# Optimization experiments

Hardware: AMD Instinct MI355X
Metric: run time of the kernel (lower is better)

Reference implementation:

```python
import jax, jax.numpy as jnp
import numpy as np

B, IN, H, OUT = 32768, 64, 256, 768
HM, TS = 4, 64  # hm_modalities, timestep_size; OUT = 3*HM*TS


def setup_inputs() -> dict:
    key = jax.random.key(0)
    ks = jax.random.split(key, 24)
    def w(k, shape):
        scale = 1.0 / np.sqrt(shape[0])
        return jax.random.normal(k, shape, jnp.float32) * scale
    inp = jax.random.normal(ks[0], (B, IN), jnp.float32)
    state1 = jax.random.normal(ks[1], (B, 2 * H), jnp.float32)
    state2 = jax.random.normal(ks[2], (B, 2 * H), jnp.float32)
    d = {"inp": inp, "state1": state1, "state2": state2}
    names = ["wf", "wk", "wi", "ws"]
    for i, n in enumerate(names):
        d[f"l1_{n}"] = w(ks[3 + i], (IN + H, H))
        d[f"l1_b{n[1]}"] = jnp.zeros((H,), jnp.float32)
        d[f"l2_{n}"] = w(ks[7 + i], (H + H, H))
        d[f"l2_b{n[1]}"] = jnp.zeros((H,), jnp.float32)
    d["ff_w"] = w(ks[11], (H, OUT))
    return d


def lstm_cell(state, x_in, wf, bf, wk, bk, wi, bi, ws, bs):
    h = wf.shape[1]
    prev_out = state[:, :h]
    cell = state[:, h:]
    x = jnp.concatenate([x_in, prev_out], axis=1)
    reset = jax.nn.sigmoid(x @ wf + bf)
    write = jax.nn.sigmoid(x @ wk + bk)
    interm = jnp.tanh(x @ wi + bi)
    read = jax.nn.sigmoid(x @ ws + bs)
    cell = reset * cell + write * interm
    out = read * jnp.tanh(cell)
    return out, jnp.concatenate([out, cell], axis=1)


def reference(inp, state1, state2,
              l1_wf, l1_bf, l1_wk, l1_bk, l1_wi, l1_bi, l1_ws, l1_bs,
              l2_wf, l2_bf, l2_wk, l2_bk, l2_wi, l2_bi, l2_ws, l2_bs,
              ff_w):
    out, new_state1 = lstm_cell(state1, inp, l1_wf, l1_bf, l1_wk, l1_bk,
                                l1_wi, l1_bi, l1_ws, l1_bs)
    out, new_state2 = lstm_cell(state2, out, l2_wf, l2_bf, l2_wk, l2_bk,
                                l2_wi, l2_bi, l2_ws, l2_bs)
    out = out @ ff_w  # [B, OUT]
    third = OUT // 3
    means = out[:, :third]
    deviances = jnp.exp(out[:, third:2 * third])
    mult = out[:, -third:].reshape(B, HM, TS)
    mult = jax.nn.softmax(mult, axis=1).reshape(B, HM * TS)
    return means, deviances, mult, new_state1, new_state2
```

## Files before the change

### kernel.cpp

```cpp
#include <hip/hip_runtime.h>


typedef __attribute__((ext_vector_type(8))) short short8;
typedef __attribute__((ext_vector_type(4))) short short4_t;
typedef __attribute__((ext_vector_type(4))) float floatx4;

#define BATCH 32768

static const size_t DEV_OFF  = (size_t)BATCH * 256;
static const size_t MULT_OFF = (size_t)2 * BATCH * 256;
static const size_t NS1_OFF  = (size_t)3 * BATCH * 256;
static const size_t NS2_OFF  = NS1_OFF + (size_t)BATCH * 512;

static const size_t W1P = 0;
static const size_t W2P = (size_t)1024 * 320;
static const size_t W3P = W2P + (size_t)1024 * 512;
static const size_t X1O = W3P + (size_t)768 * 256;
static const size_t X2O = X1O + (size_t)BATCH * 320;
static const size_t X3O = X2O + (size_t)BATCH * 512;

__device__ __forceinline__ unsigned short f2bf(float f) {
    union { float f; unsigned int i; } v; v.f = f;
    unsigned int i = v.i;
    i += 0x7fff + ((i >> 16) & 1);
    return (unsigned short)(i >> 16);
}
__device__ __forceinline__ float sigmoidf_(float x) {
    return 1.f / (1.f + __expf(-x));
}
__device__ __forceinline__ float tanhf_(float x) {
    float e = __expf(2.f * x);
    return 1.f - 2.f / (e + 1.f);
}

__device__ __forceinline__ void gl_lds16(const unsigned short* g,
                                         unsigned short* l) {
    __builtin_amdgcn_global_load_lds(
        (const __attribute__((address_space(1))) unsigned int*)g,
        (__attribute__((address_space(3))) unsigned int*)l,
        16, 0, 0);
}

__global__ __launch_bounds__(256) void pack_all(
    const float* __restrict__ inp, const float* __restrict__ s1,
    const float* __restrict__ s2,
    const float* __restrict__ w10, const float* __restrict__ w11,
    const float* __restrict__ w12, const float* __restrict__ w13,
    const float* __restrict__ w20, const float* __restrict__ w21,
    const float* __restrict__ w22, const float* __restrict__ w23,
    const float* __restrict__ fw, unsigned short* __restrict__ ws)
{
    const int q = blockIdx.x * 256 + threadIdx.x;
    if (q < 524288) {
        int r = q >> 4, c = (q & 15) << 2;
        float4 v = *(const float4*)(inp + (size_t)r * 64 + c);
        short4_t h;
        h.x = (short)f2bf(v.x); h.y = (short)f2bf(v.y);
        h.z = (short)f2bf(v.z); h.w = (short)f2bf(v.w);
        *(short4_t*)(ws + X1O + (size_t)r * 320 + c) = h;
    } else if (q < 2621440) {
        int j = q - 524288;
        int r = j >> 6, c = (j & 63) << 2;
        float4 v = *(const float4*)(s1 + (size_t)r * 512 + c);
        short4_t h;
        h.x = (short)f2bf(v.x); h.y = (short)f2bf(v.y);
        h.z = (short)f2bf(v.z); h.w = (short)f2bf(v.w);
        *(short4_t*)(ws + X1O + (size_t)r * 320 + 64 + c) = h;
    } else if (q < 4718592) {
        int j = q - 2621440;
        int r = j >> 6, c = (j & 63) << 2;
        float4 v = *(const float4*)(s2 + (size_t)r * 512 + c);
        short4_t h;
        h.x = (short)f2bf(v.x); h.y = (short)f2bf(v.y);
        h.z = (short)f2bf(v.z); h.w = (short)f2bf(v.w);
        *(short4_t*)(ws + X2O + (size_t)r * 512 + 256 + c) = h;
    } else if (q < 4800512) {
        int j = q - 4718592;
        int n = j / 80, k = (j % 80) << 2;
        int hh = ((n >> 6) << 4) + (n & 15);
        int g = (n >> 4) & 3;
        const float* s = g == 0 ? w10 : g == 1 ? w11 : g == 2 ? w12 : w13;
        short4_t o;
        o.x = (short)f2bf(s[(size_t)(k + 0) * 256 + hh]);
        o.y = (short)f2bf(s[(size_t)(k + 1) * 256 + hh]);
        o.z = (short)f2bf(s[(size_t)(k + 2) * 256 + hh]);
        o.w = (short)f2bf(s[(size_t)(k + 3) * 256 + hh]);
        *(short4_t*)(ws + W1P + (size_t)n * 320 + k) = o;
    } else if (q < 4931584) {
        int j = q - 4800512;
        int n = j >> 7, k = (j & 127) << 2;
        int hh = ((n >> 6) << 4) + (n & 15);
        int g = (n >> 4) & 3;
        const float* s = g == 0 ? w20 : g == 1 ? w21 : g == 2 ? w22 : w23;
        short4_t o;
        o.x = (short)f2bf(s[(size_t)(k + 0) * 256 + hh]);
        o.y = (short)f2bf(s[(size_t)(k + 1) * 256 + hh]);
        o.z = (short)f2bf(s[(size_t)(k + 2) * 256 + hh]);
        o.w = (short)f2bf(s[(size_t)(k + 3) * 256 + hh]);
        *(short4_t*)(ws + W2P + (size_t)n * 512 + k) = o;
    } else {
        int j = q - 4931584;
        int n = j >> 6, k = (j & 63) << 2;
        int col;
        if (n < 512) col = n;
        else {
            int t = (((n - 512) >> 6) << 4) + (n & 15);
            int m = (n >> 4) & 3;
            col = 512 + m * 64 + t;
        }
        short4_t o;
        o.x = (short)f2bf(fw[(size_t)(k + 0) * 768 + col]);
        o.y = (short)f2bf(fw[(size_t)(k + 1) * 768 + col]);
        o.z = (short)f2bf(fw[(size_t)(k + 2) * 768 + col]);
        o.w = (short)f2bf(fw[(size_t)(k + 3) * 768 + col]);
        *(short4_t*)(ws + W3P + (size_t)n * 256 + k) = o;
    }
}

template<int KT, int XST>
__global__ __launch_bounds__(256) void lstm_gemm(
    const unsigned short* __restrict__ xin,
    const unsigned short* __restrict__ wp,
    const float* __restrict__ b0, const float* __restrict__ b1,
    const float* __restrict__ b2, const float* __restrict__ b3,
    const float* __restrict__ state,
    float* __restrict__ nstate,
    unsigned short* __restrict__ xnext)
{
    __shared__ __align__(16) struct {
        unsigned short a[128][64];
        unsigned short b[128][64];
    } lds;

    const int tid  = threadIdx.x;
    const int w    = tid >> 6;
    const int lane = tid & 63;
    const int lhi  = lane >> 4, llo = lane & 15;
    const int wr   = w >> 1, wc = w & 1;

    const int lin  = blockIdx.x;
    const int xcd  = lin & 7;
    const int kk   = lin >> 3;
    const int nt   = kk & 7;
    const int row0 = (xcd * 32 + (kk >> 3)) * 128;
    const int nc0  = nt * 128;

    const int h = nt * 32 + wc * 16 + llo;
    const float bf_ = b0[h], bk_ = b1[h], bi_ = b2[h], bs_ = b3[h];

    floatx4 acc[4][4];
#pragma unroll
    for (int i = 0; i < 4; i++)
#pragma unroll
        for (int j = 0; j < 4; j++) acc[i][j] = (floatx4){0.f, 0.f, 0.f, 0.f};

    const int arow  = (w << 5) + (lane >> 3);
    const int acolb = (((lane & 7) ^ ((lane >> 3) & 7)) << 3);
    const unsigned short* agp = xin + (size_t)(row0 + arow) * KT + acolb;
    const unsigned short* bgp = wp  + (size_t)(nc0 + arow) * KT + acolb;

    const int sx  = llo & 7;
    const int kq0 = ((lhi ^ sx) << 3);
    const int kq1 = (((4 | lhi) ^ sx) << 3);

    for (int c = 0; c < KT / 64; ++c) {
        const int kb = c << 6;
#pragma unroll
        for (int p = 0; p < 4; ++p) {
            gl_lds16(agp + (size_t)(p * 8) * KT + kb,
                     &lds.a[(w << 5) + (p << 3)][0]);
            gl_lds16(bgp + (size_t)(p * 8) * KT + kb,
                     &lds.b[(w << 5) + (p << 3)][0]);
        }
        __syncthreads();
#pragma unroll
        for (int ks = 0; ks < 2; ++ks) {
            const int kq = ks ? kq1 : kq0;
            short8 a[4], b[4];
#pragma unroll
            for (int mi = 0; mi < 4; mi++)
                a[mi] = *(const short8*)&lds.a[wr * 64 + mi * 16 + llo][kq];
#pragma unroll
            for (int ni = 0; ni < 4; ni++)
                b[ni] = *(const short8*)&lds.b[wc * 64 + ni * 16 + llo][kq];
#pragma unroll
            for (int mi = 0; mi < 4; mi++)
#pragma unroll
                for (int ni = 0; ni < 4; ni++)
                    acc[mi][ni] = __builtin_amdgcn_mfma_f32_16x16x32_bf16(
                        a[mi], b[ni], acc[mi][ni], 0, 0, 0);
        }
        __syncthreads();
    }

#pragma unroll
    for (int mi = 0; mi < 4; mi++)
#pragma unroll
        for (int r = 0; r < 4; r++) {
            const int m = wr * 64 + mi * 16 + lhi * 4 + r;
            const size_t rowel = (size_t)(row0 + m) * 512;
            float rst = sigmoidf_(acc[mi][0][r] + bf_);
            float wrt = sigmoidf_(acc[mi][1][r] + bk_);
            float itm = tanhf_(acc[mi][2][r] + bi_);
            float rd  = sigmoidf_(acc[mi][3][r] + bs_);
            float cold = state[rowel + 256 + h];
            float cell = rst * cold + wrt * itm;
            float o = rd * tanhf_(cell);
            nstate[rowel + h]       = o;
            nstate[rowel + 256 + h] = cell;
            xnext[(size_t)(row0 + m) * XST + h] = f2bf(o);
        }
}

__global__ __launch_bounds__(256) void ff_gemm(
    const unsigned short* __restrict__ xin,
    const unsigned short* __restrict__ wp,
    float* __restrict__ out)
{
    __shared__ __align__(16) struct {
        unsigned short a[128][64];
        unsigned short b[128][64];
    } lds;

    const int tid  = threadIdx.x;
    const int w    = tid >> 6;
    const int lane = tid & 63;
    const int lhi  = lane >> 4, llo = lane & 15;
    const int wr   = w >> 1, wc = w & 1;

    const int lin  = blockIdx.x;
    const int xcd  = lin & 7;
    const int kk   = lin >> 3;
    const int nt   = kk % 6;
    const int row0 = (xcd * 32 + kk / 6) * 128;
    const int nc0  = nt * 128;

    floatx4 acc[4][4];
#pragma unroll
    for (int i = 0; i < 4; i++)
#pragma unroll
        for (int j = 0; j < 4; j++) acc[i][j] = (floatx4){0.f, 0.f, 0.f, 0.f};

    const int arow  = (w << 5) + (lane >> 3);
    const int acolb = (((lane & 7) ^ ((lane >> 3) & 7)) << 3);
    const unsigned short* agp = xin + (size_t)(row0 + arow) * 256 + acolb;
    const unsigned short* bgp = wp  + (size_t)(nc0 + arow) * 256 + acolb;

    const int sx  = llo & 7;
    const int kq0 = ((lhi ^ sx) << 3);
    const int kq1 = (((4 | lhi) ^ sx) << 3);

    for (int c = 0; c < 4; ++c) {
        const int kb = c << 6;
#pragma unroll
        for (int p = 0; p < 4; ++p) {
            gl_lds16(agp + (size_t)(p * 8) * 256 + kb,
                     &lds.a[(w << 5) + (p << 3)][0]);
            gl_lds16(bgp + (size_t)(p * 8) * 256 + kb,
                     &lds.b[(w << 5) + (p << 3)][0]);
        }
        __syncthreads();
#pragma unroll
        for (int ks = 0; ks < 2; ++ks) {
            const int kq = ks ? kq1 : kq0;
            short8 a[4], b[4];
#pragma unroll
            for (int mi = 0; mi < 4; mi++)
                a[mi] = *(const short8*)&lds.a[wr * 64 + mi * 16 + llo][kq];
#pragma unroll
            for (int ni = 0; ni < 4; ni++)
                b[ni] = *(const short8*)&lds.b[wc * 64 + ni * 16 + llo][kq];
#pragma unroll
            for (int mi = 0; mi < 4; mi++)
#pragma unroll
                for (int ni = 0; ni < 4; ni++)
                    acc[mi][ni] = __builtin_amdgcn_mfma_f32_16x16x32_bf16(
                        a[mi], b[ni], acc[mi][ni], 0, 0, 0);
        }
        __syncthreads();
    }

    if (nt < 4) {
        const bool dev = (nt >= 2);
        float* obase = out + (dev ? DEV_OFF : (size_t)0);
        const int cb = (nt & 1) * 128 + wc * 64;
#pragma unroll
        for (int mi = 0; mi < 4; mi++)
#pragma unroll
            for (int ni = 0; ni < 4; ni++) {
                const int cc = cb + ni * 16 + llo;
#pragma unroll
                for (int r = 0; r < 4; r++) {
                    const int m = wr * 64 + mi * 16 + lhi * 4 + r;
                    float v = acc[mi][ni][r];
                    if (dev) v = __expf(v);
                    obase[(size_t)(row0 + m) * 256 + cc] = v;
                }
            }
    } else {
        const int t = (nt - 4) * 32 + wc * 16 + llo;
#pragma unroll
        for (int mi = 0; mi < 4; mi++)
#pragma unroll
            for (int r = 0; r < 4; r++) {
                const int mrow = wr * 64 + mi * 16 + lhi * 4 + r;
                float v0 = acc[mi][0][r], v1 = acc[mi][1][r];
                float v2 = acc[mi][2][r], v3 = acc[mi][3][r];
                float mx = fmaxf(fmaxf(v0, v1), fmaxf(v2, v3));
                float e0 = __expf(v0 - mx), e1 = __expf(v1 - mx);
                float e2 = __expf(v2 - mx), e3 = __expf(v3 - mx);
                float inv = 1.f / (e0 + e1 + e2 + e3);
                size_t base = MULT_OFF + (size_t)(row0 + mrow) * 256 + t;
                out[base]       = e0 * inv;
                out[base + 64]  = e1 * inv;
                out[base + 128] = e2 * inv;
                out[base + 192] = e3 * inv;
            }
    }
}

extern "C" void kernel_launch(void* const* d_in, const int* in_sizes, int n_in,
                              void* d_out, int out_size, void* d_ws, size_t ws_size,
                              hipStream_t stream)
{
    typedef const float* cfp;
    cfp inp = (cfp)d_in[0];
    cfp st1 = (cfp)d_in[1];
    cfp st2 = (cfp)d_in[2];
    cfp l1w0 = (cfp)d_in[3],  l1w1 = (cfp)d_in[7],  l1w2 = (cfp)d_in[11], l1w3 = (cfp)d_in[15];
    cfp l1b0 = (cfp)d_in[4],  l1b1 = (cfp)d_in[8],  l1b2 = (cfp)d_in[12], l1b3 = (cfp)d_in[16];
    cfp l2w0 = (cfp)d_in[5],  l2w1 = (cfp)d_in[9],  l2w2 = (cfp)d_in[13], l2w3 = (cfp)d_in[17];
    cfp l2b0 = (cfp)d_in[6],  l2b1 = (cfp)d_in[10], l2b2 = (cfp)d_in[14], l2b3 = (cfp)d_in[18];
    cfp ffw = (cfp)d_in[19];

    float* out = (float*)d_out;
    unsigned short* ws = (unsigned short*)d_ws;

    pack_all<<<19456, 256, 0, stream>>>(inp, st1, st2,
                                        l1w0, l1w1, l1w2, l1w3,
                                        l2w0, l2w1, l2w2, l2w3, ffw, ws);

    lstm_gemm<320, 512><<<2048, 256, 0, stream>>>(
        ws + X1O, ws + W1P, l1b0, l1b1, l1b2, l1b3,
        st1, out + NS1_OFF, ws + X2O);

    lstm_gemm<512, 256><<<2048, 256, 0, stream>>>(
        ws + X2O, ws + W2P, l2b0, l2b1, l2b2, l2b3,
        st2, out + NS2_OFF, ws + X3O);

    ff_gemm<<<1536, 256, 0, stream>>>(ws + X3O, ws + W3P, out);
}
```

Baseline: 493.1 us.

## Split packing and overlap layer-2/FF packing with layer-1 GEMM via extra blocks

The single packing kernel is split in two. Layer-1 inputs and weights are packed in a smaller kernel with 4 elements per thread. Packing of state2 and the layer-2/FF weights moves into extra blocks appended to the layer-1 GEMM launch, so that conversion work can run alongside the GEMM blocks. Launch bounds of (256,4) are added to the GEMM kernels to target higher occupancy, at the risk of register spills.

Result: faster. 480.7 us (-2.5%).

```diff
diff --git a/kernel.cpp b/kernel.cpp
--- a/kernel.cpp
+++ b/kernel.cpp
@@ -41,104 +41,121 @@
         16, 0, 0);
 }
 
-__global__ __launch_bounds__(256) void pack_all(
+__global__ __launch_bounds__(256) void pack1(
     const float* __restrict__ inp, const float* __restrict__ s1,
-    const float* __restrict__ s2,
     const float* __restrict__ w10, const float* __restrict__ w11,
     const float* __restrict__ w12, const float* __restrict__ w13,
-    const float* __restrict__ w20, const float* __restrict__ w21,
-    const float* __restrict__ w22, const float* __restrict__ w23,
-    const float* __restrict__ fw, unsigned short* __restrict__ ws)
+    unsigned short* __restrict__ ws)
 {
-    const int q = blockIdx.x * 256 + threadIdx.x;
-    if (q < 524288) {
-        int r = q >> 4, c = (q & 15) << 2;
-        float4 v = *(const float4*)(inp + (size_t)r * 64 + c);
-        short4_t h;
-        h.x = (short)f2bf(v.x); h.y = (short)f2bf(v.y);
-        h.z = (short)f2bf(v.z); h.w = (short)f2bf(v.w);
-        *(short4_t*)(ws + X1O + (size_t)r * 320 + c) = h;
-    } else if (q < 2621440) {
-        int j = q - 524288;
-        int r = j >> 6, c = (j & 63) << 2;
-        float4 v = *(const float4*)(s1 + (size_t)r * 512 + c);
-        short4_t h;
-        h.x = (short)f2bf(v.x); h.y = (short)f2bf(v.y);
-        h.z = (short)f2bf(v.z); h.w = (short)f2bf(v.w);
-        *(short4_t*)(ws + X1O + (size_t)r * 320 + 64 + c) = h;
-    } else if (q < 4718592) {
-        int j = q - 2621440;
-        int r = j >> 6, c = (j & 63) << 2;
-        float4 v = *(const float4*)(s2 + (size_t)r * 512 + c);
-        short4_t h;
-        h.x = (short)f2bf(v.x); h.y = (short)f2bf(v.y);
-        h.z = (short)f2bf(v.z); h.w = (short)f2bf(v.w);
-        *(short4_t*)(ws + X2O + (size_t)r * 512 + 256 + c) = h;
-    } else if (q < 4800512) {
-        int j = q - 4718592;
-        int n = j / 80, k = (j % 80) << 2;
-        int hh = ((n >> 6) << 4) + (n & 15);
-        int g = (n >> 4) & 3;
-        const float* s = g == 0 ? w10 : g == 1 ? w11 : g == 2 ? w12 : w13;
-        short4_t o;
-        o.x = (short)f2bf(s[(size_t)(k + 0) * 256 + hh]);
-        o.y = (short)f2bf(s[(size_t)(k + 1) * 256 + hh]);
-        o.z = (short)f2bf(s[(size_t)(k + 2) * 256 + hh]);
-        o.w = (short)f2bf(s[(size_t)(k + 3) * 256 + hh]);
-        *(short4_t*)(ws + W1P + (size_t)n * 320 + k) = o;
-    } else if (q < 4931584) {
-        int j = q - 4800512;
-        int n = j >> 7, k = (j & 127) << 2;
-        int hh = ((n >> 6) << 4) + (n & 15);
-        int g = (n >> 4) & 3;
-        const float* s = g == 0 ? w20 : g == 1 ? w21 : g == 2 ? w22 : w23;
-        short4_t o;
-        o.x = (short)f2bf(s[(size_t)(k + 0) * 256 + hh]);
-        o.y = (short)f2bf(s[(size_t)(k + 1) * 256 + hh]);
-        o.z = (short)f2bf(s[(size_t)(k + 2) * 256 + hh]);
-        o.w = (short)f2bf(s[(size_t)(k + 3) * 256 + hh]);
-        *(short4_t*)(ws + W2P + (size_t)n * 512 + k) = o;
-    } else {
-        int j = q - 4931584;
-        int n = j >> 6, k = (j & 63) << 2;
-        int col;
-        if (n < 512) col = n;
-        else {
-            int t = (((n - 512) >> 6) << 4) + (n & 15);
-            int m = (n >> 4) & 3;
-            col = 512 + m * 64 + t;
-        }
-        short4_t o;
-        o.x = (short)f2bf(fw[(size_t)(k + 0) * 768 + col]);
-        o.y = (short)f2bf(fw[(size_t)(k + 1) * 768 + col]);
-        o.z = (short)f2bf(fw[(size_t)(k + 2) * 768 + col]);
-        o.w = (short)f2bf(fw[(size_t)(k + 3) * 768 + col]);
-        *(short4_t*)(ws + W3P + (size_t)n * 256 + k) = o;
-    }
-}
-
-template<int KT, int XST>
-__global__ __launch_bounds__(256) void lstm_gemm(
+    const int wt = blockIdx.x * 256 + threadIdx.x;
+#pragma unroll
+    for (int j = 0; j < 4; ++j) {
+        const int q = wt + j * 675840;
+        if (q < 524288) {
+            int r = q >> 4, c = (q & 15) << 2;
+            float4 v = *(const float4*)(inp + (size_t)r * 64 + c);
+            short4_t h;
+            h.x = (short)f2bf(v.x); h.y = (short)f2bf(v.y);
+            h.z = (short)f2bf(v.z); h.w = (short)f2bf(v.w);
+            *(short4_t*)(ws + X1O + (size_t)r * 320 + c) = h;
+        } else if (q < 2621440) {
+            int jj = q - 524288;
+            int r = jj >> 6, c = (jj & 63) << 2;
+            float4 v = *(const float4*)(s1 + (size_t)r * 512 + c);
+            short4_t h;
+            h.x = (short)f2bf(v.x); h.y = (short)f2bf(v.y);
+            h.z = (short)f2bf(v.z); h.w = (short)f2bf(v.w);
+            *(short4_t*)(ws + X1O + (size_t)r * 320 + 64 + c) = h;
+        } else {
+            int jj = q - 2621440;
+            int n = jj / 80, k = (jj % 80) << 2;
+            int hh = ((n >> 6) << 4) + (n & 15);
+            int g = (n >> 4) & 3;
+            const float* s = g == 0 ? w10 : g == 1 ? w11 : g == 2 ? w12 : w13;
+            short4_t o;
+            o.x = (short)f2bf(s[(size_t)(k + 0) * 256 + hh]);
+            o.y = (short)f2bf(s[(size_t)(k + 1) * 256 + hh]);
+            o.z = (short)f2bf(s[(size_t)(k + 2) * 256 + hh]);
+            o.w = (short)f2bf(s[(size_t)(k + 3) * 256 + hh]);
+            *(short4_t*)(ws + W1P + (size_t)n * 320 + k) = o;
+        }
+    }
+}
+
+template<int KT, int XST, bool PACK>
+__global__ __launch_bounds__(256, 4) void lstm_gemm(
     const unsigned short* __restrict__ xin,
     const unsigned short* __restrict__ wp,
     const float* __restrict__ b0, const float* __restrict__ b1,
     const float* __restrict__ b2, const float* __restrict__ b3,
     const float* __restrict__ state,
     float* __restrict__ nstate,
-    unsigned short* __restrict__ xnext)
+    unsigned short* __restrict__ xnext,
+    const float* __restrict__ s2f,
+    const float* __restrict__ w20, const float* __restrict__ w21,
+    const float* __restrict__ w22, const float* __restrict__ w23,
+    const float* __restrict__ fw,
+    unsigned short* __restrict__ wsbase)
 {
+    const int tid = threadIdx.x;
+    const int lin = blockIdx.x;
+
+    if (PACK && lin >= 2048) {
+        const int wt = (lin - 2048) * 256 + tid;
+#pragma unroll
+        for (int j = 0; j < 4; ++j) {
+            const int q = wt + j * 569344;
+            if (q < 2097152) {
+                int r = q >> 6, c = (q & 63) << 2;
+                float4 v = *(const float4*)(s2f + (size_t)r * 512 + c);
+                short4_t h;
+                h.x = (short)f2bf(v.x); h.y = (short)f2bf(v.y);
+                h.z = (short)f2bf(v.z); h.w = (short)f2bf(v.w);
+                *(short4_t*)(wsbase + X2O + (size_t)r * 512 + 256 + c) = h;
+            } else if (q < 2228224) {
+                int jj = q - 2097152;
+                int n = jj >> 7, k = (jj & 127) << 2;
+                int hh = ((n >> 6) << 4) + (n & 15);
+                int g = (n >> 4) & 3;
+                const float* s = g == 0 ? w20 : g == 1 ? w21
+                               : g == 2 ? w22 : w23;
+                short4_t o;
+                o.x = (short)f2bf(s[(size_t)(k + 0) * 256 + hh]);
+                o.y = (short)f2bf(s[(size_t)(k + 1) * 256 + hh]);
+                o.z = (short)f2bf(s[(size_t)(k + 2) * 256 + hh]);
+                o.w = (short)f2bf(s[(size_t)(k + 3) * 256 + hh]);
+                *(short4_t*)(wsbase + W2P + (size_t)n * 512 + k) = o;
+            } else {
+                int jj = q - 2228224;
+                int n = jj >> 6, k = (jj & 63) << 2;
+                int col;
+                if (n < 512) col = n;
+                else {
+                    int t = (((n - 512) >> 6) << 4) + (n & 15);
+                    int m = (n >> 4) & 3;
+                    col = 512 + m * 64 + t;
+                }
+                short4_t o;
+                o.x = (short)f2bf(fw[(size_t)(k + 0) * 768 + col]);
+                o.y = (short)f2bf(fw[(size_t)(k + 1) * 768 + col]);
+                o.z = (short)f2bf(fw[(size_t)(k + 2) * 768 + col]);
+                o.w = (short)f2bf(fw[(size_t)(k + 3) * 768 + col]);
+                *(short4_t*)(wsbase + W3P + (size_t)n * 256 + k) = o;
+            }
+        }
+        return;
+    }
+
     __shared__ __align__(16) struct {
         unsigned short a[128][64];
         unsigned short b[128][64];
     } lds;
 
-    const int tid  = threadIdx.x;
     const int w    = tid >> 6;
     const int lane = tid & 63;
     const int lhi  = lane >> 4, llo = lane & 15;
     const int wr   = w >> 1, wc = w & 1;
 
-    const int lin  = blockIdx.x;
     const int xcd  = lin & 7;
     const int kk   = lin >> 3;
     const int nt   = kk & 7;
@@ -212,7 +229,7 @@
         }
 }
 
-__global__ __launch_bounds__(256) void ff_gemm(
+__global__ __launch_bounds__(256, 4) void ff_gemm(
     const unsigned short* __restrict__ xin,
     const unsigned short* __restrict__ wp,
     float* __restrict__ out)
@@ -336,17 +353,17 @@
     float* out = (float*)d_out;
     unsigned short* ws = (unsigned short*)d_ws;
 
-    pack_all<<<19456, 256, 0, stream>>>(inp, st1, st2,
-                                        l1w0, l1w1, l1w2, l1w3,
-                                        l2w0, l2w1, l2w2, l2w3, ffw, ws);
-
-    lstm_gemm<320, 512><<<2048, 256, 0, stream>>>(
+    pack1<<<2640, 256, 0, stream>>>(inp, st1, l1w0, l1w1, l1w2, l1w3, ws);
+
+    lstm_gemm<320, 512, true><<<4272, 256, 0, stream>>>(
         ws + X1O, ws + W1P, l1b0, l1b1, l1b2, l1b3,
-        st1, out + NS1_OFF, ws + X2O);
-
-    lstm_gemm<512, 256><<<2048, 256, 0, stream>>>(
+        st1, out + NS1_OFF, ws + X2O,
+        st2, l2w0, l2w1, l2w2, l2w3, ffw, ws);
+
+    lstm_gemm<512, 256, false><<<2048, 256, 0, stream>>>(
         ws + X2O, ws + W2P, l2b0, l2b1, l2b2, l2b3,
-        st2, out + NS2_OFF, ws + X3O);
+        st2, out + NS2_OFF, ws + X3O,
+        nullptr, nullptr, nullptr, nullptr, nullptr, nullptr, nullptr);
 
     ff_gemm<<<1536, 256, 0, stream>>>(ws + X3O, ws + W3P, out);
 }
```

## Fuse fp32-to-bf16 activation conversion into LSTM GEMM A-tile loads

Applied to the files above, without the earlier changes.

Removes the separate packing pass for input and state activations: the LSTM GEMMs now read fp32 input/state directly, convert to bf16 in registers and write swizzled into LDS, while the pack kernel handles only weights. This eliminates a full read/write round trip of large bf16 staging buffers. It trades async global-to-LDS loads for synchronous register loads on those tiles, which may reduce overlap. It also adds launch_bounds occupancy hints of 4 blocks per CU.

New measurement: 522.7 us. 6.0% more time.

```diff
diff --git a/kernel.cpp b/kernel.cpp
--- a/kernel.cpp
+++ b/kernel.cpp
@@ -15,9 +15,8 @@
 static const size_t W1P = 0;
 static const size_t W2P = (size_t)1024 * 320;
 static const size_t W3P = W2P + (size_t)1024 * 512;
-static const size_t X1O = W3P + (size_t)768 * 256;
-static const size_t X2O = X1O + (size_t)BATCH * 320;
-static const size_t X3O = X2O + (size_t)BATCH * 512;
+static const size_t X2L = W3P + (size_t)768 * 256;
+static const size_t X3O = X2L + (size_t)BATCH * 256;
 
 __device__ __forceinline__ unsigned short f2bf(float f) {
     union { float f; unsigned int i; } v; v.f = f;
@@ -41,9 +40,7 @@
         16, 0, 0);
 }
 
-__global__ __launch_bounds__(256) void pack_all(
-    const float* __restrict__ inp, const float* __restrict__ s1,
-    const float* __restrict__ s2,
+__global__ __launch_bounds__(256) void pack_w(
     const float* __restrict__ w10, const float* __restrict__ w11,
     const float* __restrict__ w12, const float* __restrict__ w13,
     const float* __restrict__ w20, const float* __restrict__ w21,
@@ -51,32 +48,8 @@
     const float* __restrict__ fw, unsigned short* __restrict__ ws)
 {
     const int q = blockIdx.x * 256 + threadIdx.x;
-    if (q < 524288) {
-        int r = q >> 4, c = (q & 15) << 2;
-        float4 v = *(const float4*)(inp + (size_t)r * 64 + c);
-        short4_t h;
-        h.x = (short)f2bf(v.x); h.y = (short)f2bf(v.y);
-        h.z = (short)f2bf(v.z); h.w = (short)f2bf(v.w);
-        *(short4_t*)(ws + X1O + (size_t)r * 320 + c) = h;
-    } else if (q < 2621440) {
-        int j = q - 524288;
-        int r = j >> 6, c = (j & 63) << 2;
-        float4 v = *(const float4*)(s1 + (size_t)r * 512 + c);
-        short4_t h;
-        h.x = (short)f2bf(v.x); h.y = (short)f2bf(v.y);
-        h.z = (short)f2bf(v.z); h.w = (short)f2bf(v.w);
-        *(short4_t*)(ws + X1O + (size_t)r * 320 + 64 + c) = h;
-    } else if (q < 4718592) {
-        int j = q - 2621440;
-        int r = j >> 6, c = (j & 63) << 2;
-        float4 v = *(const float4*)(s2 + (size_t)r * 512 + c);
-        short4_t h;
-        h.x = (short)f2bf(v.x); h.y = (short)f2bf(v.y);
-        h.z = (short)f2bf(v.z); h.w = (short)f2bf(v.w);
-        *(short4_t*)(ws + X2O + (size_t)r * 512 + 256 + c) = h;
-    } else if (q < 4800512) {
-        int j = q - 4718592;
-        int n = j / 80, k = (j % 80) << 2;
+    if (q < 81920) {
+        int n = q / 80, k = (q % 80) << 2;
         int hh = ((n >> 6) << 4) + (n & 15);
         int g = (n >> 4) & 3;
         const float* s = g == 0 ? w10 : g == 1 ? w11 : g == 2 ? w12 : w13;
@@ -86,8 +59,8 @@
         o.z = (short)f2bf(s[(size_t)(k + 2) * 256 + hh]);
         o.w = (short)f2bf(s[(size_t)(k + 3) * 256 + hh]);
         *(short4_t*)(ws + W1P + (size_t)n * 320 + k) = o;
-    } else if (q < 4931584) {
-        int j = q - 4800512;
+    } else if (q < 212992) {
+        int j = q - 81920;
         int n = j >> 7, k = (j & 127) << 2;
         int hh = ((n >> 6) << 4) + (n & 15);
         int g = (n >> 4) & 3;
@@ -99,7 +72,7 @@
         o.w = (short)f2bf(s[(size_t)(k + 3) * 256 + hh]);
         *(short4_t*)(ws + W2P + (size_t)n * 512 + k) = o;
     } else {
-        int j = q - 4931584;
+        int j = q - 212992;
         int n = j >> 6, k = (j & 63) << 2;
         int col;
         if (n < 512) col = n;
@@ -117,9 +90,10 @@
     }
 }
 
-template<int KT, int XST>
-__global__ __launch_bounds__(256) void lstm_gemm(
-    const unsigned short* __restrict__ xin,
+template<int KT, bool L1>
+__global__ __launch_bounds__(256, 4) void lstm_gemm(
+    const float* __restrict__ f32x,
+    const unsigned short* __restrict__ xbf,
     const unsigned short* __restrict__ wp,
     const float* __restrict__ b0, const float* __restrict__ b1,
     const float* __restrict__ b2, const float* __restrict__ b3,
@@ -156,8 +130,14 @@
 
     const int arow  = (w << 5) + (lane >> 3);
     const int acolb = (((lane & 7) ^ ((lane >> 3) & 7)) << 3);
-    const unsigned short* agp = xin + (size_t)(row0 + arow) * KT + acolb;
-    const unsigned short* bgp = wp  + (size_t)(nc0 + arow) * KT + acolb;
+    const unsigned short* bgp = wp + (size_t)(nc0 + arow) * KT + acolb;
+    const unsigned short* agp =
+        L1 ? nullptr : xbf + (size_t)(row0 + arow) * 256 + acolb;
+
+    const int r0  = tid >> 4;
+    const int c4  = (tid & 15) << 2;
+    const int chk = c4 >> 3;
+    const int hlf = c4 & 7;
 
     const int sx  = llo & 7;
     const int kq0 = ((lhi ^ sx) << 3);
@@ -166,11 +146,38 @@
     for (int c = 0; c < KT / 64; ++c) {
         const int kb = c << 6;
 #pragma unroll
-        for (int p = 0; p < 4; ++p) {
-            gl_lds16(agp + (size_t)(p * 8) * KT + kb,
-                     &lds.a[(w << 5) + (p << 3)][0]);
+        for (int p = 0; p < 4; ++p)
             gl_lds16(bgp + (size_t)(p * 8) * KT + kb,
                      &lds.b[(w << 5) + (p << 3)][0]);
+        if (!L1 && c < 4) {
+#pragma unroll
+            for (int p = 0; p < 4; ++p)
+                gl_lds16(agp + (size_t)(p * 8) * 256 + kb,
+                         &lds.a[(w << 5) + (p << 3)][0]);
+        } else {
+            const float* src; int sstr, scol;
+            if (L1) {
+                if (c == 0) { src = f32x;  sstr = 64;  scol = 0; }
+                else        { src = state; sstr = 512; scol = (c - 1) * 64; }
+            } else          { src = state; sstr = 512; scol = (c - 4) * 64; }
+#pragma unroll
+            for (int g2 = 0; g2 < 2; ++g2) {
+                float4 v[4];
+#pragma unroll
+                for (int qq = 0; qq < 4; ++qq) {
+                    const int r = r0 + (g2 * 4 + qq) * 16;
+                    v[qq] = *(const float4*)(src + (size_t)(row0 + r) * sstr
+                                             + scol + c4);
+                }
+#pragma unroll
+                for (int qq = 0; qq < 4; ++qq) {
+                    const int r = r0 + (g2 * 4 + qq) * 16;
+                    short4_t hh;
+                    hh.x = (short)f2bf(v[qq].x); hh.y = (short)f2bf(v[qq].y);
+                    hh.z = (short)f2bf(v[qq].z); hh.w = (short)f2bf(v[qq].w);
+                    *(short4_t*)&lds.a[r][((chk ^ (r & 7)) << 3) + hlf] = hh;
+                }
+            }
         }
         __syncthreads();
 #pragma unroll
@@ -208,11 +215,11 @@
             float o = rd * tanhf_(cell);
             nstate[rowel + h]       = o;
             nstate[rowel + 256 + h] = cell;
-            xnext[(size_t)(row0 + m) * XST + h] = f2bf(o);
-        }
-}
-
-__global__ __launch_bounds__(256) void ff_gemm(
+            xnext[(size_t)(row0 + m) * 256 + h] = f2bf(o);
+        }
+}
+
+__global__ __launch_bounds__(256, 4) void ff_gemm(
     const unsigned short* __restrict__ xin,
     const unsigned short* __restrict__ wp,
     float* __restrict__ out)
@@ -336,16 +343,15 @@
     float* out = (float*)d_out;
     unsigned short* ws = (unsigned short*)d_ws;
 
-    pack_all<<<19456, 256, 0, stream>>>(inp, st1, st2,
-                                        l1w0, l1w1, l1w2, l1w3,
-                                        l2w0, l2w1, l2w2, l2w3, ffw, ws);
-
-    lstm_gemm<320, 512><<<2048, 256, 0, stream>>>(
-        ws + X1O, ws + W1P, l1b0, l1b1, l1b2, l1b3,
-        st1, out + NS1_OFF, ws + X2O);
-
-    lstm_gemm<512, 256><<<2048, 256, 0, stream>>>(
-        ws + X2O, ws + W2P, l2b0, l2b1, l2b2, l2b3,
+    pack_w<<<1024, 256, 0, stream>>>(l1w0, l1w1, l1w2, l1w3,
+                                     l2w0, l2w1, l2w2, l2w3, ffw, ws);
+
+    lstm_gemm<320, true><<<2048, 256, 0, stream>>>(
+        inp, nullptr, ws + W1P, l1b0, l1b1, l1b2, l1b3,
+        st1, out + NS1_OFF, ws + X2L);
+
+    lstm_gemm<512, false><<<2048, 256, 0, stream>>>(
+        nullptr, ws + X2L, ws + W2P, l2b0, l2b1, l2b2, l2b3,
         st2, out + NS2_OFF, ws + X3O);
 
     ff_gemm<<<1536, 256, 0, stream>>>(ws + X3O, ws + W3P, out);
```
